# Kernel optimization log

Hardware: AMD Instinct MI355X
Metric: run time of the kernel (lower is better)

## Reference

```python
import jax, jax.numpy as jnp
import numpy as np
import math

Z, N_CTX, D, D_FF = 64, 2048, 64, 32
NEG = -1e9  # finite stand-in for -inf additive mask (avoids NaN rows)
EPS = 1e-5


def _layer_norm(y):
    # LayerNorm without affine params, matching F.layer_norm / the kernel math
    mu = jnp.mean(y, axis=-1, keepdims=True)
    yc = y - mu
    var = jnp.mean(yc * yc, axis=-1, keepdims=True)
    return yc / jnp.sqrt(var + EPS)


def setup_inputs() -> dict:
    key = jax.random.key(0)
    ks = jax.random.split(key, 7)
    x = jax.random.normal(ks[0], (Z, N_CTX, D), dtype=jnp.float32)
    scale = 1.0 / math.sqrt(D)
    q = jax.random.normal(ks[1], (D, D), dtype=jnp.float32) * scale
    k = jax.random.normal(ks[2], (D, D), dtype=jnp.float32) * scale
    v = jax.random.normal(ks[3], (D, D), dtype=jnp.float32) * scale
    w1 = jax.random.normal(ks[4], (D, D_FF), dtype=jnp.float32) * scale
    w2 = jax.random.normal(ks[5], (D_FF, D), dtype=jnp.float32) * (1.0 / math.sqrt(D_FF))
    # additive masks: 0 = keep, NEG = masked
    key_padding_mask = jnp.zeros((Z, N_CTX), dtype=jnp.float32)
    causal_mask = jnp.triu(jnp.full((N_CTX, N_CTX), NEG, dtype=jnp.float32), k=1)
    return {"x": x, "q": q, "k": k, "v": v, "w1": w1, "w2": w2,
            "key_padding_mask": key_padding_mask, "causal_mask": causal_mask}


def reference(x, q, k, v, w1, w2, key_padding_mask, causal_mask):
    sm_scale = 1.0 / math.sqrt(D)
    # QKV projections (single head)
    Q = jnp.einsum('bnd,de->bne', x, q)
    K = jnp.einsum('bnd,de->bne', x, k)
    V = jnp.einsum('bnd,de->bne', x, v)
    # attention scores; kernel adds masks BEFORE scaling: (QK^T + kpm + cm) * sm_scale
    scores = jnp.einsum('bid,bjd->bij', Q, K)
    scores = (scores + key_padding_mask[:, None, :] + causal_mask[None, :, :]) * sm_scale
    p = jax.nn.softmax(scores, axis=-1)
    attn = jnp.einsum('bij,bjd->bid', p, V)
    # residual + LN (no affine)
    y = _layer_norm(attn + x)
    # FFN: relu(y @ w1) @ w2, residual, LN
    h = jax.nn.relu(jnp.einsum('bnd,df->bnf', y, w1))
    ff = jnp.einsum('bnf,fd->bnd', h, w2)
    out = _layer_norm(ff + y)
    return out
```

## Files before the change

### kernel.cpp

```cpp
#include <hip/hip_runtime.h>
#include <cstdint>
#include <cstddef>


#define ZB   64
#define NCTX 2048
#define DH   64
#define DFF  32
#define SC2   0.18033688011112042f
#define NEGS2 (-1.8033688e8f)

typedef float f32x4  __attribute__((ext_vector_type(4)));
typedef float f32x16 __attribute__((ext_vector_type(16)));
typedef __bf16 bf16x8 __attribute__((ext_vector_type(8)));
typedef unsigned int u32x4 __attribute__((ext_vector_type(4)));

#define MFMA32(a, b, c) __builtin_amdgcn_mfma_f32_32x32x16_bf16((a), (b), (c), 0, 0, 0)

static __device__ __forceinline__ unsigned cvtpk_bf16(float a, float b) {
  unsigned r;
  asm("v_cvt_pk_bf16_f32 %0, %1, %2" : "=v"(r) : "v"(a), "v"(b));
  return r;
}
static __device__ __forceinline__ void plswap32(unsigned &a, unsigned &b) {
  asm volatile("v_permlane32_swap_b32 %0, %1" : "+v"(a), "+v"(b));
}
static __device__ __forceinline__ float exp2a(float x) {
  float r;
  asm("v_exp_f32 %0, %1" : "=v"(r) : "v"(x));
  return r;
}
static __device__ __forceinline__ float redsum32(float v) {
  return v + __shfl_xor(v, 32);
}
static __device__ __forceinline__ bf16x8 pack_frag(
    float v0, float v1, float v2, float v3,
    float v4, float v5, float v6, float v7) {
  unsigned A0 = cvtpk_bf16(v0, v1), A1 = cvtpk_bf16(v2, v3);
  unsigned B0 = cvtpk_bf16(v4, v5), B1 = cvtpk_bf16(v6, v7);
  plswap32(A0, B0); plswap32(A1, B1);
  u32x4 u = {A0, A1, B0, B1};
  return __builtin_bit_cast(bf16x8, u);
}

__global__ __launch_bounds__(256) void proj_kernel(
    const float* __restrict__ x, const float* __restrict__ wq,
    const float* __restrict__ wk, const float* __restrict__ wv,
    const float* __restrict__ w1, const float* __restrict__ w2,
    const float* __restrict__ kpm,
    __bf16* __restrict__ Qp, __bf16* __restrict__ Kp, __bf16* __restrict__ Vp,
    float* __restrict__ kpmS, __bf16* __restrict__ w1p, __bf16* __restrict__ w2p)
{
  const int wid = threadIdx.x >> 6;
  const int l   = threadIdx.x & 63;
  const int q5  = l & 31, hi = l >> 5;
  const int tile = blockIdx.x * 4 + wid;
  const int b   = tile >> 6;
  const int tk  = tile & 63;
  const int n   = (tk << 5) + q5;

  __shared__ float vtile[4][32][67];

  if (blockIdx.x == 0 && wid == 0) {
    #pragma unroll
    for (int kk = 0; kk < 4; ++kk)
      #pragma unroll
      for (int i = 0; i < 8; ++i)
        w1p[(kk * 64 + l) * 8 + i] = (__bf16)w1[(16 * kk + 8 * hi + i) * DFF + q5];
    #pragma unroll
    for (int dt = 0; dt < 2; ++dt)
      #pragma unroll
      for (int kk2 = 0; kk2 < 2; ++kk2)
        #pragma unroll
        for (int i = 0; i < 8; ++i)
          w2p[((dt * 2 + kk2) * 64 + l) * 8 + i] =
              (__bf16)w2[(16 * kk2 + 8 * hi + i) * DH + 32 * dt + q5];
  }
  if (hi == 0) kpmS[b * NCTX + n] = kpm[b * NCTX + n] * SC2;

  const float* xr = x + ((size_t)(b * NCTX + n)) * DH + 8 * hi;
  bf16x8 xb[4];
  #pragma unroll
  for (int kk = 0; kk < 4; ++kk) {
    const f32x4 a = *(const f32x4*)(xr + 16 * kk);
    const f32x4 c = *(const f32x4*)(xr + 16 * kk + 4);
    u32x4 u = {cvtpk_bf16(a[0], a[1]), cvtpk_bf16(a[2], a[3]),
               cvtpk_bf16(c[0], c[1]), cvtpk_bf16(c[2], c[3])};
    xb[kk] = __builtin_bit_cast(bf16x8, u);
  }

  const size_t tbase = ((size_t)(b * 64 + tk)) * 2048;

  #pragma unroll
  for (int m = 0; m < 3; ++m) {
    const float* w = (m == 0) ? wq : (m == 1) ? wk : wv;

    f32x16 c0, c1;
    #pragma unroll
    for (int r = 0; r < 16; ++r) { c0[r] = 0.f; c1[r] = 0.f; }

    #pragma unroll
    for (int kk = 0; kk < 4; ++kk) {
      const float* wp = w + (size_t)(16 * kk + 8 * hi) * DH + q5;
      float f0[8], f1[8];
      #pragma unroll
      for (int i = 0; i < 8; ++i) { f0[i] = wp[i * DH]; f1[i] = wp[i * DH + 32]; }
      u32x4 ua = {cvtpk_bf16(f0[0], f0[1]), cvtpk_bf16(f0[2], f0[3]),
                  cvtpk_bf16(f0[4], f0[5]), cvtpk_bf16(f0[6], f0[7])};
      u32x4 ub = {cvtpk_bf16(f1[0], f1[1]), cvtpk_bf16(f1[2], f1[3]),
                  cvtpk_bf16(f1[4], f1[5]), cvtpk_bf16(f1[6], f1[7])};
      c0 = MFMA32(__builtin_bit_cast(bf16x8, ua), xb[kk], c0);
      c1 = MFMA32(__builtin_bit_cast(bf16x8, ub), xb[kk], c1);
    }

    if (m == 0) {
      #pragma unroll
      for (int r = 0; r < 16; ++r) { c0[r] *= SC2; c1[r] *= SC2; }
    }

    if (m < 2) {
      __bf16* dst = ((m == 0) ? Qp : Kp) + tbase;
      #pragma unroll
      for (int g = 0; g < 4; ++g) {
        unsigned A0 = cvtpk_bf16(c0[4 * g],     c0[4 * g + 1]);
        unsigned A1 = cvtpk_bf16(c0[4 * g + 2], c0[4 * g + 3]);
        unsigned B0 = cvtpk_bf16(c1[4 * g],     c1[4 * g + 1]);
        unsigned B1 = cvtpk_bf16(c1[4 * g + 2], c1[4 * g + 3]);
        plswap32(A0, B0); plswap32(A1, B1);
        u32x4 u = {A0, A1, B0, B1};
        const int c    = 2 * hi + (g >> 1);
        const int slot = ((g & 1) << 5) + q5;
        *(u32x4*)(dst + ((size_t)c * 64 + slot) * 8) = u;
      }
    } else {
      #pragma unroll
      for (int r = 0; r < 16; ++r) {
        const int d = (r & 3) + 8 * (r >> 2) + 4 * hi;
        vtile[wid][q5][d]      = c0[r];
        vtile[wid][q5][d + 32] = c1[r];
      }
      asm volatile("s_waitcnt lgkmcnt(0)" ::: "memory");
      __builtin_amdgcn_sched_barrier(0);
      __bf16* vdst = Vp + tbase + (size_t)l * 8;
      #pragma unroll
      for (int f = 0; f < 4; ++f) {
        const int krow = 16 * (f & 1) + 8 * hi;
        const int dcol = q5 + 32 * (f >> 1);
        u32x4 u;
        #pragma unroll
        for (int ii = 0; ii < 4; ++ii)
          u[ii] = cvtpk_bf16(vtile[wid][krow + 2 * ii][dcol],
                             vtile[wid][krow + 2 * ii + 1][dcol]);
        *(u32x4*)(vdst + (size_t)f * 512) = u;
      }
    }
  }
}

static __device__ __forceinline__ void attn_phase(
    const __bf16* __restrict__ qt,
    const __bf16* __restrict__ kB,
    const __bf16* __restrict__ vB,
    const float*  __restrict__ kpb,
    int T, int j0, int j1, int q5, int hi,
    f32x16& acc0, f32x16& acc1, float& lsq)
{
  if (j0 >= j1) return;

  const bf16x8 qf0 = *(const bf16x8*)(qt);
  const bf16x8 qf1 = *(const bf16x8*)(qt + 512);
  const bf16x8 qf2 = *(const bf16x8*)(qt + 1024);
  const bf16x8 qf3 = *(const bf16x8*)(qt + 1536);

  f32x16 z16;
  #pragma unroll
  for (int r = 0; r < 16; ++r) z16[r] = 0.f;

  bf16x8 kA0, kA1, kA2, kA3, kB0, kB1, kB2, kB3;
  {
    const __bf16* kp = kB + (size_t)j0 * 2048;
    kA0 = *(const bf16x8*)(kp);        kA1 = *(const bf16x8*)(kp + 512);
    kA2 = *(const bf16x8*)(kp + 1024); kA3 = *(const bf16x8*)(kp + 1536);
  }
  int j = j0;

#define ATTN_ITER(KC0, KC1, KC2, KC3, KN0, KN1, KN2, KN3)                   \
  {                                                                         \
    const bool last = (j + 1 >= j1);                                        \
    const bool dg = last && (j1 == T);                                      \
    const __bf16* vp = vB + (size_t)j * 2048;                               \
    const bf16x8 vf0 = *(const bf16x8*)(vp);                                \
    const bf16x8 vf1 = *(const bf16x8*)(vp + 512);                          \
    const bf16x8 vf2 = *(const bf16x8*)(vp + 1024);                         \
    const bf16x8 vf3 = *(const bf16x8*)(vp + 1536);                         \
    const float* kp2 = kpb + j * 32 + 4 * hi;                               \
    f32x4 km[4];                                                            \
    km[0] = *(const f32x4*)(kp2);      km[1] = *(const f32x4*)(kp2 + 8);    \
    km[2] = *(const f32x4*)(kp2 + 16); km[3] = *(const f32x4*)(kp2 + 24);   \
    if (!last) {                                                            \
      const __bf16* kp = kB + (size_t)(j + 1) * 2048;                       \
      KN0 = *(const bf16x8*)(kp);        KN1 = *(const bf16x8*)(kp + 512);  \
      KN2 = *(const bf16x8*)(kp + 1024); KN3 = *(const bf16x8*)(kp + 1536); \
    }                                                                       \
    __builtin_amdgcn_s_setprio(1);                                          \
    f32x16 s = MFMA32(KC0, qf0, z16);                                       \
    s = MFMA32(KC1, qf1, s);                                                \
    s = MFMA32(KC2, qf2, s);                                                \
    s = MFMA32(KC3, qf3, s);                                                \
    __builtin_amdgcn_s_setprio(0);                                          \
    float p[16];                                                            \
    if (dg) {                                                               \
      _Pragma("unroll")                                                     \
      for (int r = 0; r < 16; ++r) {                                        \
        const int rm = (r & 3) + 8 * (r >> 2) + 4 * hi;                     \
        const float tv = s[r] + km[r >> 2][r & 3] + ((rm > q5) ? NEGS2 : 0.f); \
        p[r] = exp2a(tv);                                                   \
      }                                                                     \
    } else {                                                                \
      _Pragma("unroll")                                                     \
      for (int r = 0; r < 16; ++r) p[r] = exp2a(s[r] + km[r >> 2][r & 3]);  \
    }                                                                       \
    lsq += ((p[0] + p[1]) + (p[2] + p[3])) + ((p[4] + p[5]) + (p[6] + p[7]))  \
         + ((p[8] + p[9]) + (p[10] + p[11])) + ((p[12] + p[13]) + (p[14] + p[15])); \
    const bf16x8 pf0 = pack_frag(p[0], p[1], p[2],  p[3],  p[4],  p[5],  p[6],  p[7]);  \
    const bf16x8 pf1 = pack_frag(p[8], p[9], p[10], p[11], p[12], p[13], p[14], p[15]); \
    __builtin_amdgcn_s_setprio(1);                                          \
    acc0 = MFMA32(vf0, pf0, acc0);                                          \
    acc0 = MFMA32(vf1, pf1, acc0);                                          \
    acc1 = MFMA32(vf2, pf0, acc1);                                          \
    acc1 = MFMA32(vf3, pf1, acc1);                                          \
    __builtin_amdgcn_s_setprio(0);                                          \
  }

  for (;;) {
    ATTN_ITER(kA0, kA1, kA2, kA3, kB0, kB1, kB2, kB3);
    if (++j >= j1) break;
    ATTN_ITER(kB0, kB1, kB2, kB3, kA0, kA1, kA2, kA3);
    if (++j >= j1) break;
  }
#undef ATTN_ITER
}

__global__ __launch_bounds__(128) void fused_kernel(
    const __bf16* __restrict__ Qp, const __bf16* __restrict__ Kp,
    const __bf16* __restrict__ Vp, const float* __restrict__ kpmS,
    const float* __restrict__ x,
    const __bf16* __restrict__ w1p, const __bf16* __restrict__ w2p,
    float* __restrict__ out)
{
  const int bid = (blockIdx.x & 7) * 256 + (blockIdx.x >> 3);
  const int b   = bid >> 5;
  const int tp  = bid & 31;
  const int wv  = threadIdx.x >> 6;
  const int l   = threadIdx.x & 63;
  const int q5  = l & 31;
  const int hi  = l >> 5;

  const int t1 = tp, t2 = 63 - tp;

  __shared__ float part[2][64][36];

  const __bf16* qB = Qp + (size_t)b * (64 * 2048) + (size_t)l * 8;
  const __bf16* kB = Kp + (size_t)b * (64 * 2048) + (size_t)l * 8;
  const __bf16* vB = Vp + (size_t)b * (64 * 2048) + (size_t)l * 8;
  const float*  kpb = kpmS + b * NCTX;

  f32x16 acc0, acc1;
  float lsq;
  #pragma unroll
  for (int r = 0; r < 16; ++r) { acc0[r] = 0.f; acc1[r] = 0.f; }
  lsq = 0.f;

  #pragma unroll
  for (int ph = 0; ph < 2; ++ph) {
    const int t = (wv ^ ph) ? t2 : t1;
    const int T = t + 1;
    const int h = (T + 1) >> 1;
    const int j0 = wv ? h : 0;
    const int j1 = wv ? T : h;
    attn_phase(qB + (size_t)t * 2048, kB, vB, kpb,
               T, j0, j1, q5, hi, acc0, acc1, lsq);
    if (ph == 0) {
      float* ps = &part[wv][l][0];
      #pragma unroll
      for (int g = 0; g < 4; ++g) {
        f32x4 t0, t1v;
        #pragma unroll
        for (int jj = 0; jj < 4; ++jj) { t0[jj] = acc0[4 * g + jj]; t1v[jj] = acc1[4 * g + jj]; }
        *(f32x4*)(ps + 4 * g)      = t0;
        *(f32x4*)(ps + 16 + 4 * g) = t1v;
      }
      ps[32] = lsq;
      #pragma unroll
      for (int r = 0; r < 16; ++r) { acc0[r] = 0.f; acc1[r] = 0.f; }
      lsq = 0.f;
    }
  }
  const int tB = wv ? t1 : t2;

  __syncthreads();

  {
    const float* po = &part[wv ^ 1][l][0];
    #pragma unroll
    for (int g = 0; g < 4; ++g) {
      const f32x4 t0 = *(const f32x4*)(po + 4 * g);
      const f32x4 t1v = *(const f32x4*)(po + 16 + 4 * g);
      #pragma unroll
      for (int jj = 0; jj < 4; ++jj) { acc0[4 * g + jj] += t0[jj]; acc1[4 * g + jj] += t1v[jj]; }
    }
    lsq += po[32];
  }

  const int n = tB * 32 + q5;
  const float invl = 1.f / redsum32(lsq);
  const float* xrow = x + ((size_t)(b * NCTX + n)) * DH;

  f32x16 z16;
  #pragma unroll
  for (int r = 0; r < 16; ++r) z16[r] = 0.f;

  float y0[16], y1[16];
  float s1 = 0.f, s2 = 0.f;
  #pragma unroll
  for (int g = 0; g < 4; ++g) {
    const f32x4 xv0 = *(const f32x4*)(xrow + 8 * g + 4 * hi);
    const f32x4 xv1 = *(const f32x4*)(xrow + 32 + 8 * g + 4 * hi);
    #pragma unroll
    for (int jj = 0; jj < 4; ++jj) {
      const float a0 = acc0[4 * g + jj] * invl + xv0[jj];
      const float a1 = acc1[4 * g + jj] * invl + xv1[jj];
      y0[4 * g + jj] = a0; y1[4 * g + jj] = a1;
      s1 += a0 + a1; s2 += a0 * a0 + a1 * a1;
    }
  }
  s1 = redsum32(s1);
  s2 = redsum32(s2);
  {
    const float mu   = s1 * (1.f / 64.f);
    const float var  = s2 * (1.f / 64.f) - mu * mu;
    const float rstd = rsqrtf(var + 1e-5f);
    #pragma unroll
    for (int r = 0; r < 16; ++r) {
      y0[r] = (y0[r] - mu) * rstd;
      y1[r] = (y1[r] - mu) * rstd;
    }
  }

  const bf16x8 yb0 = pack_frag(y0[0], y0[1], y0[2],  y0[3],  y0[4],  y0[5],  y0[6],  y0[7]);
  const bf16x8 yb1 = pack_frag(y0[8], y0[9], y0[10], y0[11], y0[12], y0[13], y0[14], y0[15]);
  const bf16x8 yb2 = pack_frag(y1[0], y1[1], y1[2],  y1[3],  y1[4],  y1[5],  y1[6],  y1[7]);
  const bf16x8 yb3 = pack_frag(y1[8], y1[9], y1[10], y1[11], y1[12], y1[13], y1[14], y1[15]);

  const __bf16* wp1 = w1p + (size_t)l * 8;
  f32x16 hc;
  hc = MFMA32(*(const bf16x8*)(wp1),              yb0, z16);
  hc = MFMA32(*(const bf16x8*)(wp1 + 64 * 8),     yb1, hc);
  hc = MFMA32(*(const bf16x8*)(wp1 + 2 * 64 * 8), yb2, hc);
  hc = MFMA32(*(const bf16x8*)(wp1 + 3 * 64 * 8), yb3, hc);
  float hv[16];
  #pragma unroll
  for (int r = 0; r < 16; ++r) hv[r] = fmaxf(hc[r], 0.f);

  const bf16x8 hb0 = pack_frag(hv[0], hv[1], hv[2],  hv[3],  hv[4],  hv[5],  hv[6],  hv[7]);
  const bf16x8 hb1 = pack_frag(hv[8], hv[9], hv[10], hv[11], hv[12], hv[13], hv[14], hv[15]);

  const __bf16* wp2 = w2p + (size_t)l * 8;
  f32x16 f20, f21;
  f20 = MFMA32(*(const bf16x8*)(wp2),              hb0, z16);
  f20 = MFMA32(*(const bf16x8*)(wp2 + 64 * 8),     hb1, f20);
  f21 = MFMA32(*(const bf16x8*)(wp2 + 2 * 64 * 8), hb0, z16);
  f21 = MFMA32(*(const bf16x8*)(wp2 + 3 * 64 * 8), hb1, f21);

  float v1 = 0.f, v2 = 0.f;
  float va0[16], va1[16];
  #pragma unroll
  for (int r = 0; r < 16; ++r) {
    va0[r] = f20[r] + y0[r];
    va1[r] = f21[r] + y1[r];
    v1 += va0[r] + va1[r];
    v2 += va0[r] * va0[r] + va1[r] * va1[r];
  }
  v1 = redsum32(v1);
  v2 = redsum32(v2);
  const float mu2   = v1 * (1.f / 64.f);
  const float var2  = v2 * (1.f / 64.f) - mu2 * mu2;
  const float rstd2 = rsqrtf(var2 + 1e-5f);

  float* op = out + ((size_t)(b * NCTX + n)) * DH + 4 * hi;
  #pragma unroll
  for (int g = 0; g < 4; ++g) {
    f32x4 st0, st1;
    #pragma unroll
    for (int jj = 0; jj < 4; ++jj) {
      st0[jj] = (va0[4 * g + jj] - mu2) * rstd2;
      st1[jj] = (va1[4 * g + jj] - mu2) * rstd2;
    }
    *(f32x4*)(op + 8 * g)      = st0;
    *(f32x4*)(op + 32 + 8 * g) = st1;
  }
}

extern "C" void kernel_launch(void* const* d_in, const int* in_sizes, int n_in,
                              void* d_out, int out_size, void* d_ws, size_t ws_size,
                              hipStream_t stream)
{
  const float* x   = (const float*)d_in[0];
  const float* wq  = (const float*)d_in[1];
  const float* wk  = (const float*)d_in[2];
  const float* wv  = (const float*)d_in[3];
  const float* w1  = (const float*)d_in[4];
  const float* w2  = (const float*)d_in[5];
  const float* kpm = (const float*)d_in[6];
  float* out = (float*)d_out;

  char* ws = (char*)d_ws;
  const size_t nelem = (size_t)ZB * NCTX * DH;
  __bf16* Qp   = (__bf16*)(ws);
  __bf16* Kp   = (__bf16*)(ws + nelem * 2);
  __bf16* Vp   = (__bf16*)(ws + nelem * 4);
  float*  kpmS = (float*)(ws + nelem * 6);
  __bf16* w1p  = (__bf16*)(ws + nelem * 6 + (size_t)ZB * NCTX * 4);
  __bf16* w2p  = w1p + 4 * 64 * 8;

  proj_kernel <<<1024, 256, 0, stream>>>(x, wq, wk, wv, w1, w2, kpm,
                                         Qp, Kp, Vp, kpmS, w1p, w2p);
  fused_kernel<<<ZB * 32, 128, 0, stream>>>(Qp, Kp, Vp, kpmS, x, w1p, w2p, out);
}
```

Before: 104.6 us.

## Software-pipeline attention loop: overlap next QK MFMA with current softmax-PV

Restructures the attention inner loop so the QK^T MFMA for tile j+1 is issued before the exp/PV work for tile j, using two score accumulators in ping-pong. The key-padding mask is loaded directly into the score accumulator as the MFMA initial value, which removes the separate mask add. K and mask prefetch now run two tiles ahead. This is meant to hide MFMA latency behind the exp and pack work, at the cost of more registers for the second score tile.

```diff
diff --git a/kernel.cpp b/kernel.cpp
--- a/kernel.cpp
+++ b/kernel.cpp
@@ -159,8 +159,8 @@
 
 static __device__ __forceinline__ void attn_phase(
     const __bf16* __restrict__ qt,
-    const __bf16* __restrict__ kB,
-    const __bf16* __restrict__ vB,
+    const __bf16* __restrict__ kBp,
+    const __bf16* __restrict__ vBp,
     const float*  __restrict__ kpb,
     int T, int j0, int j1, int q5, int hi,
     f32x16& acc0, f32x16& acc1, float& lsq)
@@ -172,53 +172,58 @@
   const bf16x8 qf2 = *(const bf16x8*)(qt + 1024);
   const bf16x8 qf3 = *(const bf16x8*)(qt + 1536);
 
-  f32x16 z16;
-  #pragma unroll
-  for (int r = 0; r < 16; ++r) z16[r] = 0.f;
-
   bf16x8 kA0, kA1, kA2, kA3, kB0, kB1, kB2, kB3;
-  {
-    const __bf16* kp = kB + (size_t)j0 * 2048;
-    kA0 = *(const bf16x8*)(kp);        kA1 = *(const bf16x8*)(kp + 512);
-    kA2 = *(const bf16x8*)(kp + 1024); kA3 = *(const bf16x8*)(kp + 1536);
-  }
-  int j = j0;
-
-#define ATTN_ITER(KC0, KC1, KC2, KC3, KN0, KN1, KN2, KN3)                   \
-  {                                                                         \
-    const bool last = (j + 1 >= j1);                                        \
-    const bool dg = last && (j1 == T);                                      \
-    const __bf16* vp = vB + (size_t)j * 2048;                               \
-    const bf16x8 vf0 = *(const bf16x8*)(vp);                                \
-    const bf16x8 vf1 = *(const bf16x8*)(vp + 512);                          \
-    const bf16x8 vf2 = *(const bf16x8*)(vp + 1024);                         \
-    const bf16x8 vf3 = *(const bf16x8*)(vp + 1536);                         \
-    const float* kp2 = kpb + j * 32 + 4 * hi;                               \
-    f32x4 km[4];                                                            \
-    km[0] = *(const f32x4*)(kp2);      km[1] = *(const f32x4*)(kp2 + 8);    \
-    km[2] = *(const f32x4*)(kp2 + 16); km[3] = *(const f32x4*)(kp2 + 24);   \
-    if (!last) {                                                            \
-      const __bf16* kp = kB + (size_t)(j + 1) * 2048;                       \
-      KN0 = *(const bf16x8*)(kp);        KN1 = *(const bf16x8*)(kp + 512);  \
-      KN2 = *(const bf16x8*)(kp + 1024); KN3 = *(const bf16x8*)(kp + 1536); \
+  f32x16 sA, sB;
+
+#define LOADK(P0, P1, P2, P3, J) do {                                       \
+    const __bf16* _kp = kBp + (size_t)(J) * 2048;                           \
+    P0 = *(const bf16x8*)(_kp);        P1 = *(const bf16x8*)(_kp + 512);    \
+    P2 = *(const bf16x8*)(_kp + 1024); P3 = *(const bf16x8*)(_kp + 1536);   \
+  } while (0)
+
+#define KMLD(S, J) do {                                                     \
+    const float* _mp = kpb + (J) * 32 + 4 * hi;                             \
+    const f32x4 _m0 = *(const f32x4*)(_mp);                                 \
+    const f32x4 _m1 = *(const f32x4*)(_mp + 8);                             \
+    const f32x4 _m2 = *(const f32x4*)(_mp + 16);                            \
+    const f32x4 _m3 = *(const f32x4*)(_mp + 24);                            \
+    _Pragma("unroll")                                                       \
+    for (int _jj = 0; _jj < 4; ++_jj) {                                     \
+      S[_jj] = _m0[_jj];      S[4 + _jj] = _m1[_jj];                        \
+      S[8 + _jj] = _m2[_jj];  S[12 + _jj] = _m3[_jj];                       \
     }                                                                       \
+  } while (0)
+
+#define QKP(S, P0, P1, P2, P3) do {                                         \
     __builtin_amdgcn_s_setprio(1);                                          \
-    f32x16 s = MFMA32(KC0, qf0, z16);                                       \
-    s = MFMA32(KC1, qf1, s);                                                \
-    s = MFMA32(KC2, qf2, s);                                                \
-    s = MFMA32(KC3, qf3, s);                                                \
+    S = MFMA32(P0, qf0, S);                                                 \
+    S = MFMA32(P1, qf1, S);                                                 \
+    S = MFMA32(P2, qf2, S);                                                 \
+    S = MFMA32(P3, qf3, S);                                                 \
     __builtin_amdgcn_s_setprio(0);                                          \
+  } while (0)
+
+#define CONSUME(S, J, DG, PF, PK0, PK1, PK2, PK3) do {                      \
+    const __bf16* _vp = vBp + (size_t)(J) * 2048;                           \
+    const bf16x8 vf0 = *(const bf16x8*)(_vp);                               \
+    const bf16x8 vf1 = *(const bf16x8*)(_vp + 512);                         \
+    const bf16x8 vf2 = *(const bf16x8*)(_vp + 1024);                        \
+    const bf16x8 vf3 = *(const bf16x8*)(_vp + 1536);                        \
     float p[16];                                                            \
-    if (dg) {                                                               \
+    if (DG) {                                                               \
       _Pragma("unroll")                                                     \
       for (int r = 0; r < 16; ++r) {                                        \
         const int rm = (r & 3) + 8 * (r >> 2) + 4 * hi;                     \
-        const float tv = s[r] + km[r >> 2][r & 3] + ((rm > q5) ? NEGS2 : 0.f); \
-        p[r] = exp2a(tv);                                                   \
+        p[r] = exp2a((rm > q5) ? S[r] + NEGS2 : S[r]);                      \
       }                                                                     \
     } else {                                                                \
       _Pragma("unroll")                                                     \
-      for (int r = 0; r < 16; ++r) p[r] = exp2a(s[r] + km[r >> 2][r & 3]);  \
+      for (int r = 0; r < 16; ++r) p[r] = exp2a(S[r]);                      \
+    }                                                                       \
+    if (PF) {                                                               \
+      const int _jn = ((J) + 2 < j1) ? (J) + 2 : j1 - 1;                    \
+      LOADK(PK0, PK1, PK2, PK3, _jn);                                       \
+      KMLD(S, _jn);                                                         \
     }                                                                       \
     lsq += ((p[0] + p[1]) + (p[2] + p[3])) + ((p[4] + p[5]) + (p[6] + p[7]))  \
          + ((p[8] + p[9]) + (p[10] + p[11])) + ((p[12] + p[13]) + (p[14] + p[15])); \
@@ -230,15 +235,32 @@
     acc1 = MFMA32(vf2, pf0, acc1);                                          \
     acc1 = MFMA32(vf3, pf1, acc1);                                          \
     __builtin_amdgcn_s_setprio(0);                                          \
-  }
-
-  for (;;) {
-    ATTN_ITER(kA0, kA1, kA2, kA3, kB0, kB1, kB2, kB3);
-    if (++j >= j1) break;
-    ATTN_ITER(kB0, kB1, kB2, kB3, kA0, kA1, kA2, kA3);
-    if (++j >= j1) break;
-  }
-#undef ATTN_ITER
+  } while (0)
+
+  LOADK(kA0, kA1, kA2, kA3, j0);
+  KMLD(sA, j0);
+  QKP(sA, kA0, kA1, kA2, kA3);
+  if (j1 - j0 == 1) {
+    CONSUME(sA, j0, (j1 == T), false, kB0, kB1, kB2, kB3);
+  } else {
+    LOADK(kB0, kB1, kB2, kB3, j0 + 1);
+    KMLD(sB, j0 + 1);
+    int j = j0;
+    for (;;) {
+      QKP(sB, kB0, kB1, kB2, kB3);
+      CONSUME(sA, j, false, true, kA0, kA1, kA2, kA3);
+      ++j;
+      if (j + 1 >= j1) { CONSUME(sB, j, (j1 == T), false, kA0, kA1, kA2, kA3); break; }
+      QKP(sA, kA0, kA1, kA2, kA3);
+      CONSUME(sB, j, false, true, kB0, kB1, kB2, kB3);
+      ++j;
+      if (j + 1 >= j1) { CONSUME(sA, j, (j1 == T), false, kB0, kB1, kB2, kB3); break; }
+    }
+  }
+#undef LOADK
+#undef KMLD
+#undef QKP
+#undef CONSUME
 }
 
 __global__ __launch_bounds__(128) void fused_kernel(
```

Result: faster. 97.42 us (-6.8%).
